# Kernel tuning notes

Measured on AMD Instinct MI355X. Metric: run time of the kernel, lower is better.

## Reference

```python
import jax, jax.numpy as jnp
import numpy as np

B, S, D, H = 8, 2048, 1024, 8
HD = D // H


def _linear_params(key, d_in, d_out):
    kw, kb = jax.random.split(key)
    w = jax.random.normal(kw, (d_out, d_in), jnp.float32) * 0.02
    b = jax.random.normal(kb, (d_out,), jnp.float32) * 0.02
    return w, b


def setup_inputs() -> dict:
    key = jax.random.key(0)
    ks = jax.random.split(key, 16)
    inp = {}
    inp['input_seq'] = jax.random.normal(ks[0], (B, S, D), jnp.float32)
    inp['output_seq'] = jax.random.normal(ks[1], (B, S, D), jnp.float32)
    # PositionalEncoding parameter: sin(arange(D) / 10000 ** (arange(D)/D))
    ar = jnp.arange(D, dtype=jnp.float32)
    inp['pe'] = jnp.sin(ar / 10000.0 ** (ar / D))
    names = ['enc_wq enc_bq', 'enc_wk enc_bk', 'enc_wv enc_bv',
             'enc_w1 enc_b1', 'enc_w2 enc_b2',
             'dec_s_wq dec_s_bq', 'dec_s_wk dec_s_bk', 'dec_s_wv dec_s_bv',
             'dec_c_wq dec_c_bq', 'dec_c_wk dec_c_bk', 'dec_c_wv dec_c_bv',
             'dec_w1 dec_b1', 'dec_w2 dec_b2', 'fc_w fc_b']
    for i, pair in enumerate(names):
        wn, bn = pair.split()
        w, b = _linear_params(ks[2 + i], D, D)
        inp[wn], inp[bn] = w, b
    return inp


def _mha(q_in, k_in, wq, bq, wk, bk, wv, bv):
    # Faithful to source: head split WITHOUT transpose -> per-position 8x8 head mixing.
    q = (q_in @ wq.T + bq).reshape(q_in.shape[0], q_in.shape[1], H, HD)
    k = (k_in @ wk.T + bk).reshape(k_in.shape[0], k_in.shape[1], H, HD)
    v = (k_in @ wv.T + bv).reshape(k_in.shape[0], k_in.shape[1], H, HD)
    scores = jnp.einsum('bsih,bsjh->bsij', q, k) / jnp.sqrt(jnp.float32(HD))
    w = jax.nn.softmax(scores, axis=-1)  # dropout before softmax is identity at eval
    out = jnp.einsum('bsij,bsjh->bsih', w, v)
    return out.reshape(q_in.shape[0], q_in.shape[1], -1)


def reference(input_seq, output_seq, pe,
              enc_wq, enc_bq, enc_wk, enc_bk, enc_wv, enc_bv,
              enc_w1, enc_b1, enc_w2, enc_b2,
              dec_s_wq, dec_s_bq, dec_s_wk, dec_s_bk, dec_s_wv, dec_s_bv,
              dec_c_wq, dec_c_bq, dec_c_wk, dec_c_bk, dec_c_wv, dec_c_bv,
              dec_w1, dec_b1, dec_w2, dec_b2, fc_w, fc_b):
    x = input_seq + pe  # additive positional encoding
    # encoder layer
    a = _mha(x, x, enc_wq, enc_bq, enc_wk, enc_bk, enc_wv, enc_bv)
    enc_out = jax.nn.relu(a @ enc_w1.T + enc_b1) @ enc_w2.T + enc_b2
    # decoder layer (training branch: output_seq given)
    sa = _mha(output_seq, output_seq, dec_s_wq, dec_s_bq, dec_s_wk, dec_s_bk, dec_s_wv, dec_s_bv)
    ca = _mha(sa, enc_out, dec_c_wq, dec_c_bq, dec_c_wk, dec_c_bk, dec_c_wv, dec_c_bv)
    dec_out = jax.nn.relu(ca @ dec_w1.T + dec_b1) @ dec_w2.T + dec_b2
    return dec_out @ fc_w.T + fc_b
```

## Files before the change

### kernel.cpp

```cpp
#include <hip/hip_runtime.h>
#include <stdint.h>


#define TOKENS 16384
#define DMODEL 1024

typedef unsigned short ushort_t;
typedef __attribute__((ext_vector_type(8))) short short8;
typedef __attribute__((ext_vector_type(4))) float floatx4;

__device__ __forceinline__ float b2f(ushort_t u) {
  union { uint32_t i; float f; } v; v.i = ((uint32_t)u) << 16; return v.f;
}
__device__ __forceinline__ ushort_t f2b(float f) {
  union { float f; uint32_t i; } v; v.f = f;
  uint32_t r = v.i + 0x7fffu + ((v.i >> 16) & 1u);
  return (ushort_t)(r >> 16);
}

__device__ __forceinline__ void pack8(const float* __restrict__ g, ushort_t* dst) {
  float4 x = *(const float4*)g;
  float4 y = *(const float4*)(g + 4);
  ushort_t o[8] = {f2b(x.x), f2b(x.y), f2b(x.z), f2b(x.w),
                   f2b(y.x), f2b(y.y), f2b(y.z), f2b(y.w)};
  *(uint4*)dst = *(uint4*)o;
}

#define GLD16(g, l)                                                          \
  __builtin_amdgcn_global_load_lds(                                          \
      (const __attribute__((address_space(1))) void*)(g),                    \
      (__attribute__((address_space(3))) void*)(l), 16, 0, 0)

struct ConvArgs {
  const float* src[14];
  ushort_t* dst[14];
};

__global__ __launch_bounds__(256) void conv_w_kernel(ConvArgs a) {
  const int w = blockIdx.y;
  const int idx = (blockIdx.x * 256 + threadIdx.x) * 8;
  pack8(a.src[w] + idx, a.dst[w] + idx);
}

__global__ __launch_bounds__(256) void conv_x_kernel(
    const float* __restrict__ src, ushort_t* __restrict__ dst) {
  const int idx = (blockIdx.x * 256 + threadIdx.x) * 8;
  pack8(src + idx, dst + idx);
}

__global__ __launch_bounds__(256) void add_pe_kernel(
    const float* __restrict__ in, const float* __restrict__ pe,
    ushort_t* __restrict__ out) {
  int idx = (blockIdx.x * 256 + threadIdx.x) * 8;
  int d = idx & (DMODEL - 1);
  float4 a0 = *(const float4*)(in + idx);
  float4 a1 = *(const float4*)(in + idx + 4);
  float4 p0 = *(const float4*)(pe + d);
  float4 p1 = *(const float4*)(pe + d + 4);
  ushort_t o[8] = {f2b(a0.x + p0.x), f2b(a0.y + p0.y), f2b(a0.z + p0.z), f2b(a0.w + p0.w),
                   f2b(a1.x + p1.x), f2b(a1.y + p1.y), f2b(a1.z + p1.z), f2b(a1.w + p1.w)};
  *(uint4*)(out + idx) = *(uint4*)o;
}

template <int D, int MH>
__device__ __forceinline__ void load_a(const ushort_t* sA, int aoff, int cs0,
                                       int cs1, short8 (&af)[4][2]) {
  const ushort_t* p = sA + D * 16384 + MH * 8192 + aoff;
#pragma unroll
  for (int i = 0; i < 4; i++) {
    af[i][0] = *(const short8*)&p[i * 1024 + cs0];
    af[i][1] = *(const short8*)&p[i * 1024 + cs1];
  }
}

template <int D, int NH>
__device__ __forceinline__ void load_b(const ushort_t* sB, int boff, int cs0,
                                       int cs1, short8 (&bf)[2][2]) {
  const ushort_t* p = sB + D * 16384 + NH * 8192 + boff;
#pragma unroll
  for (int j = 0; j < 2; j++) {
    bf[j][0] = *(const short8*)&p[j * 1024 + cs0];
    bf[j][1] = *(const short8*)&p[j * 1024 + cs1];
  }
}

template <int QA, int QB>
__device__ __forceinline__ void mfma_region(floatx4 (&acc)[4][4][2],
                                            const short8 (&af)[4][2],
                                            const short8 (&b0)[2][2],
                                            const short8 (&b1)[2][2]) {
  __builtin_amdgcn_s_setprio(1);
#pragma unroll
  for (int i = 0; i < 4; i++)
#pragma unroll
    for (int j = 0; j < 2; j++) {
      acc[QA][i][j] = __builtin_amdgcn_mfma_f32_16x16x32_bf16(
          af[i][0], b0[j][0], acc[QA][i][j], 0, 0, 0);
      acc[QA][i][j] = __builtin_amdgcn_mfma_f32_16x16x32_bf16(
          af[i][1], b0[j][1], acc[QA][i][j], 0, 0, 0);
    }
#pragma unroll
  for (int i = 0; i < 4; i++)
#pragma unroll
    for (int j = 0; j < 2; j++) {
      acc[QB][i][j] = __builtin_amdgcn_mfma_f32_16x16x32_bf16(
          af[i][0], b1[j][0], acc[QB][i][j], 0, 0, 0);
      acc[QB][i][j] = __builtin_amdgcn_mfma_f32_16x16x32_bf16(
          af[i][1], b1[j][1], acc[QB][i][j], 0, 0, 0);
    }
  __builtin_amdgcn_s_setprio(0);
}

#define BARRIER_PINNED                                                       \
  do {                                                                       \
    __builtin_amdgcn_sched_barrier(0);                                       \
    __builtin_amdgcn_s_barrier();                                            \
    __builtin_amdgcn_sched_barrier(0);                                       \
  } while (0)

#define STAGE_A(h, tk, d)                                                    \
  do {                                                                       \
    GLD16(gA + (size_t)((h) * 131072 + (tk) * 64),                           \
          sA + (d) * 16384 + (h) * 8192 + lo);                               \
    GLD16(gA + (size_t)((h) * 131072 + 65536 + (tk) * 64),                   \
          sA + (d) * 16384 + (h) * 8192 + 4096 + lo);                        \
  } while (0)
#define STAGE_B(h, tk, d)                                                    \
  do {                                                                       \
    GLD16(gB + (size_t)((h) * 131072 + (tk) * 64),                           \
          sB + (d) * 16384 + (h) * 8192 + lo);                               \
    GLD16(gB + (size_t)((h) * 131072 + 65536 + (tk) * 64),                   \
          sB + (d) * 16384 + (h) * 8192 + 4096 + lo);                        \
  } while (0)

#define GROUP(tt, dd)                                                        \
  do {                                                                       \
    load_a<dd, 0>(sA, aoff, cs0, cs1, af);                                   \
    load_b<dd, 0>(sB, boff, cs0, cs1, bf0);                                  \
    load_b<dd, 1>(sB, boff, cs0, cs1, bf1);                                  \
    if ((tt) + 1 < NT) {                                                     \
      STAGE_B(0, (tt) + 1, (dd) ^ 1);                                        \
      STAGE_A(1, (tt) + 1, (dd) ^ 1);                                        \
    }                                                                        \
    mfma_region<0, 1>(acc, af, bf0, bf1);                                    \
    asm volatile("s_waitcnt lgkmcnt(0)");                                    \
    BARRIER_PINNED;                                                          \
    load_a<dd, 1>(sA, aoff, cs0, cs1, af);                                   \
    if ((tt) + 2 < NT) {                                                     \
      STAGE_A(0, (tt) + 2, dd);                                              \
      STAGE_B(1, (tt) + 2, dd);                                              \
    }                                                                        \
    mfma_region<2, 3>(acc, af, bf0, bf1);                                    \
    if ((tt) + 2 < NT)                                                       \
      asm volatile("s_waitcnt vmcnt(4) lgkmcnt(0)");                         \
    else if ((tt) + 1 < NT)                                                  \
      asm volatile("s_waitcnt vmcnt(0) lgkmcnt(0)");                         \
    else                                                                     \
      asm volatile("s_waitcnt lgkmcnt(0)");                                  \
    BARRIER_PINNED;                                                          \
  } while (0)

template <bool RELU, bool OUT32>
__global__ __launch_bounds__(512, 2) void gemm_bt(
    const ushort_t* __restrict__ A, const ushort_t* __restrict__ W,
    const float* __restrict__ bias, void* __restrict__ Cp) {
  constexpr int K = 1024, N = 1024, NT = 16;
  extern __shared__ ushort_t smem[];
  ushort_t* sA = smem;
  ushort_t* sB = smem + 32768;

  const int tid = threadIdx.x;
  const int lane = tid & 63;
  const int wid = tid >> 6;

  const int orig = blockIdx.x;
  const int swz = (orig & 7) * 32 + (orig >> 3);
  const int m0 = (swz >> 2) * 256;
  const int n0 = (swz & 3) * 256;

  const int qm = (wid >> 2) * 64;
  const int qn = (wid & 3) * 32;
  const int lr = lane & 15;
  const int lq = lane >> 4;
  const int xr = lane & 7;
  const int cs0 = (lq ^ xr) * 8;
  const int cs1 = ((4 + lq) ^ xr) * 8;
  const int aoff = (qm + lr) * 64;
  const int boff = (qn + lr) * 64;

  const int rl = tid >> 3;
  const int j8 = tid & 7;
  const int co = (j8 ^ (rl & 7)) * 8;
  const int lo = tid * 8;
  const ushort_t* gA = A + (size_t)(m0 + rl) * K + co;
  const ushort_t* gB = W + (size_t)(n0 + rl) * K + co;

  floatx4 acc[4][4][2] = {};
  short8 af[4][2], bf0[2][2], bf1[2][2];

  STAGE_A(0, 0, 0);
  STAGE_B(1, 0, 0);
  STAGE_B(0, 0, 0);
  STAGE_A(1, 0, 0);
  STAGE_A(0, 1, 1);
  STAGE_B(1, 1, 1);
  asm volatile("s_waitcnt vmcnt(4)");
  BARRIER_PINNED;

#pragma unroll 1
  for (int t = 0; t < NT; t += 2) {
    GROUP(t, 0);
    GROUP(t + 1, 1);
  }

  const int rbase = lq * 4;

  if constexpr (OUT32) {
    float* sCf = (float*)smem;
#pragma unroll
    for (int p = 0; p < 4; p++) {
      if ((qm >> 6) == (p & 1)) {
#pragma unroll
        for (int Nh = 0; Nh < 2; Nh++)
#pragma unroll
          for (int j = 0; j < 2; j++) {
            const int col = Nh * 128 + qn + j * 16 + lr;
            const float bv = bias[n0 + col];
#pragma unroll
            for (int i = 0; i < 4; i++)
#pragma unroll
              for (int r = 0; r < 4; r++) {
                float v = acc[(p >> 1) * 2 + Nh][i][j][r] + bv;
                if (RELU) v = fmaxf(v, 0.0f);
                sCf[(i * 16 + rbase + r) * 260 + col] = v;
              }
          }
      }
      __syncthreads();
#pragma unroll
      for (int u = 0; u < 8; u++) {
        const int lin = u * 512 + tid;
        const int row = lin >> 6;
        const int c4 = (lin & 63) * 4;
        *(float4*)((float*)Cp + (size_t)(m0 + p * 64 + row) * N + n0 + c4) =
            *(const float4*)&sCf[row * 260 + c4];
      }
      __syncthreads();
    }
    return;
  }

  ushort_t* sC = smem;
#pragma unroll
  for (int p = 0; p < 2; p++) {
#pragma unroll
    for (int Nh = 0; Nh < 2; Nh++)
#pragma unroll
      for (int j = 0; j < 2; j++) {
        const int col = Nh * 128 + qn + j * 16 + lr;
        const float bv = bias[n0 + col];
#pragma unroll
        for (int i = 0; i < 4; i++)
#pragma unroll
          for (int r = 0; r < 4; r++) {
            float v = acc[p * 2 + Nh][i][j][r] + bv;
            if (RELU) v = fmaxf(v, 0.0f);
            sC[(qm + i * 16 + rbase + r) * 264 + col] = f2b(v);
          }
      }
    __syncthreads();
#pragma unroll
    for (int u = 0; u < 8; u++) {
      const int lin = u * 512 + tid;
      const int row = lin >> 5;
      const int c8 = (lin & 31) * 8;
      *(uint4*)((ushort_t*)Cp + (size_t)(m0 + p * 128 + row) * N + n0 + c8) =
          *(const uint4*)&sC[row * 264 + c8];
    }
    __syncthreads();
  }
}

__global__ __launch_bounds__(256) void attn_kernel(
    const ushort_t* Q, const ushort_t* Kp, const ushort_t* Vp, ushort_t* O) {
  __shared__ __align__(16) ushort_t sq[4][1024];
  __shared__ __align__(16) ushort_t sk[4][1024];
  __shared__ __align__(16) ushort_t sv[4][1024];
  __shared__ float sp[4][64];

  const int t = threadIdx.x;
  const int w = t >> 6;
  const int lane = t & 63;
  const size_t base = ((size_t)blockIdx.x * 4 + w) * 1024;

  ((uint4*)sq[w])[lane] = ((const uint4*)(Q + base))[lane];
  ((uint4*)sq[w])[lane + 64] = ((const uint4*)(Q + base))[lane + 64];
  ((uint4*)sk[w])[lane] = ((const uint4*)(Kp + base))[lane];
  ((uint4*)sk[w])[lane + 64] = ((const uint4*)(Kp + base))[lane + 64];
  ((uint4*)sv[w])[lane] = ((const uint4*)(Vp + base))[lane];
  ((uint4*)sv[w])[lane + 64] = ((const uint4*)(Vp + base))[lane + 64];
  __syncthreads();

  {
    const int i = lane >> 3, j = lane & 7;
    const ushort_t* qr = &sq[w][i * 128];
    const ushort_t* kr = &sk[w][j * 128];
    float s = 0.0f;
#pragma unroll 16
    for (int h = 0; h < 128; h++) s += b2f(qr[h]) * b2f(kr[h]);
    s *= 0.08838834764831845f;
    float m = s;
#pragma unroll
    for (int off = 1; off < 8; off <<= 1) m = fmaxf(m, __shfl_xor(m, off, 64));
    float e = __expf(s - m);
    float sum = e;
#pragma unroll
    for (int off = 1; off < 8; off <<= 1) sum += __shfl_xor(sum, off, 64);
    sp[w][lane] = e / sum;
  }
  __syncthreads();

  {
    const int i = lane >> 3;
    const int hb = (lane & 7) * 16;
    float p[8];
#pragma unroll
    for (int jj = 0; jj < 8; jj++) p[jj] = sp[w][i * 8 + jj];
    float o[16];
#pragma unroll
    for (int h = 0; h < 16; h++) {
      float acc = 0.0f;
#pragma unroll
      for (int jj = 0; jj < 8; jj++) acc += p[jj] * b2f(sv[w][jj * 128 + hb + h]);
      o[h] = acc;
    }
    uint32_t packed[8];
#pragma unroll
    for (int u = 0; u < 8; u++)
      packed[u] = (uint32_t)f2b(o[2 * u]) | ((uint32_t)f2b(o[2 * u + 1]) << 16);
    uint4* dst = (uint4*)(O + base + i * 128 + hb);
    dst[0] = *(uint4*)&packed[0];
    dst[1] = *(uint4*)&packed[4];
  }
}

extern "C" void kernel_launch(void* const* d_in, const int* in_sizes, int n_in,
                              void* d_out, int out_size, void* d_ws, size_t ws_size,
                              hipStream_t stream) {
  const float* input_seq = (const float*)d_in[0];
  const float* output_seq = (const float*)d_in[1];
  const float* pe = (const float*)d_in[2];
  const float* wsrc[14] = {
      (const float*)d_in[3],  (const float*)d_in[5],  (const float*)d_in[7],
      (const float*)d_in[9],  (const float*)d_in[11], (const float*)d_in[13],
      (const float*)d_in[15], (const float*)d_in[17], (const float*)d_in[19],
      (const float*)d_in[21], (const float*)d_in[23], (const float*)d_in[25],
      (const float*)d_in[27], (const float*)d_in[29]};
  const float* enc_bq = (const float*)d_in[4];
  const float* enc_bk = (const float*)d_in[6];
  const float* enc_bv = (const float*)d_in[8];
  const float* enc_b1 = (const float*)d_in[10];
  const float* enc_b2 = (const float*)d_in[12];
  const float* dsq_b = (const float*)d_in[14];
  const float* dsk_b = (const float*)d_in[16];
  const float* dsv_b = (const float*)d_in[18];
  const float* dcq_b = (const float*)d_in[20];
  const float* dck_b = (const float*)d_in[22];
  const float* dcv_b = (const float*)d_in[24];
  const float* dec_b1 = (const float*)d_in[26];
  const float* dec_b2 = (const float*)d_in[28];
  const float* fc_b = (const float*)d_in[30];

  const size_t SZ = (size_t)TOKENS * DMODEL;
  const size_t WSZ = (size_t)DMODEL * DMODEL;
  ushort_t* bA = (ushort_t*)d_ws;
  ushort_t* bB = bA + SZ;
  ushort_t* oseq = bB + SZ;
  ushort_t* wts = oseq + SZ;
  ushort_t* oL = (ushort_t*)d_out;
  ushort_t* oH = oL + SZ;
  float* outf = (float*)d_out;

  static bool attr_set = false;
  if (!attr_set) {
    (void)hipFuncSetAttribute(reinterpret_cast<const void*>(&gemm_bt<false, false>),
                              hipFuncAttributeMaxDynamicSharedMemorySize, 131072);
    (void)hipFuncSetAttribute(reinterpret_cast<const void*>(&gemm_bt<true, false>),
                              hipFuncAttributeMaxDynamicSharedMemorySize, 131072);
    (void)hipFuncSetAttribute(reinterpret_cast<const void*>(&gemm_bt<false, true>),
                              hipFuncAttributeMaxDynamicSharedMemorySize, 131072);
    attr_set = true;
  }

  ConvArgs ca;
#pragma unroll
  for (int i = 0; i < 14; i++) { ca.src[i] = wsrc[i]; ca.dst[i] = wts + (size_t)i * WSZ; }

  const dim3 gG(TOKENS / 256 * (DMODEL / 256));
  const dim3 gblk(512);
  const dim3 blk(256);
  const int LDSB = 131072;
  const int gPE = TOKENS * DMODEL / (256 * 8);
  const int gAT = TOKENS / 4;

  conv_w_kernel<<<dim3(WSZ / (256 * 8), 14), blk, 0, stream>>>(ca);
  conv_x_kernel<<<gPE, blk, 0, stream>>>(output_seq, oseq);
  add_pe_kernel<<<gPE, blk, 0, stream>>>(input_seq, pe, bA);
  gemm_bt<false, false><<<gG, gblk, LDSB, stream>>>(bA, wts + 0 * WSZ, enc_bq, bB);
  gemm_bt<false, false><<<gG, gblk, LDSB, stream>>>(bA, wts + 1 * WSZ, enc_bk, oL);
  gemm_bt<false, false><<<gG, gblk, LDSB, stream>>>(bA, wts + 2 * WSZ, enc_bv, oH);
  attn_kernel<<<gAT, blk, 0, stream>>>(bB, oL, oH, bB);
  gemm_bt<true, false><<<gG, gblk, LDSB, stream>>>(bB, wts + 3 * WSZ, enc_b1, bA);
  gemm_bt<false, false><<<gG, gblk, LDSB, stream>>>(bA, wts + 4 * WSZ, enc_b2, bB);
  gemm_bt<false, false><<<gG, gblk, LDSB, stream>>>(oseq, wts + 5 * WSZ, dsq_b, bA);
  gemm_bt<false, false><<<gG, gblk, LDSB, stream>>>(oseq, wts + 6 * WSZ, dsk_b, oL);
  gemm_bt<false, false><<<gG, gblk, LDSB, stream>>>(oseq, wts + 7 * WSZ, dsv_b, oH);
  attn_kernel<<<gAT, blk, 0, stream>>>(bA, oL, oH, bA);
  gemm_bt<false, false><<<gG, gblk, LDSB, stream>>>(bA, wts + 8 * WSZ, dcq_b, oL);
  gemm_bt<false, false><<<gG, gblk, LDSB, stream>>>(bB, wts + 9 * WSZ, dck_b, oH);
  gemm_bt<false, false><<<gG, gblk, LDSB, stream>>>(bB, wts + 10 * WSZ, dcv_b, bA);
  attn_kernel<<<gAT, blk, 0, stream>>>(oL, oH, bA, oL);
  gemm_bt<true, false><<<gG, gblk, LDSB, stream>>>(oL, wts + 11 * WSZ, dec_b1, bB);
  gemm_bt<false, false><<<gG, gblk, LDSB, stream>>>(bB, wts + 12 * WSZ, dec_b2, bA);
  gemm_bt<false, true><<<gG, gblk, LDSB, stream>>>(bA, wts + 13 * WSZ, fc_b, outf);
}
```

Before: 822.9 us.

## Simplify GEMM pipeline to single barrier per k-tile with full-tile prefetch

Replaces the split-phase prefetch schedule, which issued half of the next tile and half of the tile after across two barriers per k-step, with a plain double buffer. All four half-tiles of the next k-tile are issued at once and there is one vmcnt(0) wait and barrier per step. The sched_barrier pinning is replaced by a plain asm s_barrier with a memory clobber. This halves barrier count but loses the two-deep lookahead and the fine-grained vmcnt overlap, so global loads may be exposed more.

```diff
diff --git a/kernel.cpp b/kernel.cpp
--- a/kernel.cpp
+++ b/kernel.cpp
@@ -111,12 +111,7 @@
   __builtin_amdgcn_s_setprio(0);
 }
 
-#define BARRIER_PINNED                                                       \
-  do {                                                                       \
-    __builtin_amdgcn_sched_barrier(0);                                       \
-    __builtin_amdgcn_s_barrier();                                            \
-    __builtin_amdgcn_sched_barrier(0);                                       \
-  } while (0)
+#define BARSB asm volatile("s_barrier" ::: "memory")
 
 #define STAGE_A(h, tk, d)                                                    \
   do {                                                                       \
@@ -139,25 +134,16 @@
     load_b<dd, 0>(sB, boff, cs0, cs1, bf0);                                  \
     load_b<dd, 1>(sB, boff, cs0, cs1, bf1);                                  \
     if ((tt) + 1 < NT) {                                                     \
+      STAGE_A(0, (tt) + 1, (dd) ^ 1);                                        \
       STAGE_B(0, (tt) + 1, (dd) ^ 1);                                        \
       STAGE_A(1, (tt) + 1, (dd) ^ 1);                                        \
+      STAGE_B(1, (tt) + 1, (dd) ^ 1);                                        \
     }                                                                        \
     mfma_region<0, 1>(acc, af, bf0, bf1);                                    \
-    asm volatile("s_waitcnt lgkmcnt(0)");                                    \
-    BARRIER_PINNED;                                                          \
     load_a<dd, 1>(sA, aoff, cs0, cs1, af);                                   \
-    if ((tt) + 2 < NT) {                                                     \
-      STAGE_A(0, (tt) + 2, dd);                                              \
-      STAGE_B(1, (tt) + 2, dd);                                              \
-    }                                                                        \
     mfma_region<2, 3>(acc, af, bf0, bf1);                                    \
-    if ((tt) + 2 < NT)                                                       \
-      asm volatile("s_waitcnt vmcnt(4) lgkmcnt(0)");                         \
-    else if ((tt) + 1 < NT)                                                  \
-      asm volatile("s_waitcnt vmcnt(0) lgkmcnt(0)");                         \
-    else                                                                     \
-      asm volatile("s_waitcnt lgkmcnt(0)");                                  \
-    BARRIER_PINNED;                                                          \
+    asm volatile("s_waitcnt vmcnt(0) lgkmcnt(0)" ::: "memory");              \
+    BARSB;                                                                   \
   } while (0)
 
 template <bool RELU, bool OUT32>
@@ -199,13 +185,11 @@
   short8 af[4][2], bf0[2][2], bf1[2][2];
 
   STAGE_A(0, 0, 0);
-  STAGE_B(1, 0, 0);
   STAGE_B(0, 0, 0);
   STAGE_A(1, 0, 0);
-  STAGE_A(0, 1, 1);
-  STAGE_B(1, 1, 1);
-  asm volatile("s_waitcnt vmcnt(4)");
-  BARRIER_PINNED;
+  STAGE_B(1, 0, 0);
+  asm volatile("s_waitcnt vmcnt(0)" ::: "memory");
+  BARSB;
 
 #pragma unroll 1
   for (int t = 0; t < NT; t += 2) {
```

Measured after the change: 829.6 us. Within noise of the previous version (+0.8%).
